# Optimization experiments

Measured on AMD Instinct MI355X. Metric: run time of the kernel, lower is better.

The kernel has to match this reference:

```python
import jax, jax.numpy as jnp
import numpy as np

B, N, L, C, H = 4, 4096, 1024, 1024, 16
D = C // H  # head_dim = 64
SCALE = 1.0 / np.sqrt(D)


def setup_inputs() -> dict:
    key = jax.random.key(0)
    ks = jax.random.split(key, 5)
    return {
        "x": jax.random.normal(ks[0], (B, N, C), dtype=jnp.float32),
        "query": jax.random.normal(ks[1], (B, L, C), dtype=jnp.float32),
        "Wq": jax.random.normal(ks[2], (C, C), dtype=jnp.float32) * 0.02,
        "Wkv": jax.random.normal(ks[3], (2 * C, C), dtype=jnp.float32) * 0.02,
        "Wproj": jax.random.normal(ks[4], (C, C), dtype=jnp.float32) * 0.02,
        "bproj": jnp.zeros((C,), dtype=jnp.float32),
    }


def reference(x, query, Wq, Wkv, Wproj, bproj):
    # q projection: [B,L,C] -> [B,H,L,D]
    q = (query @ Wq.T).reshape(B, L, H, D).transpose(0, 2, 1, 3)
    # kv projection: [B,N,2C] -> k,v each [B,H,N,D]
    kv = (x @ Wkv.T).reshape(B, N, 2, H, D).transpose(2, 0, 3, 1, 4)
    k, v = kv[0], kv[1]
    # unfused SDPA: explicit [B,H,L,N] score matrix (faithful to source)
    attn = jnp.einsum('bhld,bhnd->bhln', q, k) * SCALE
    attn = jax.nn.softmax(attn, axis=-1)
    out = jnp.einsum('bhln,bhnd->bhld', attn, v)  # [B,H,L,D]
    out = out.transpose(0, 2, 1, 3).reshape(B, L, C)
    return out @ Wproj.T + bproj
```

## Files before the change

### kernel.cpp

```cpp
#include <hip/hip_runtime.h>
#include <hip/hip_bf16.h>

typedef __attribute__((ext_vector_type(8))) short short8;
typedef __attribute__((ext_vector_type(4))) float floatx4;

#if __has_builtin(__builtin_amdgcn_exp2f)
#define EXP2(x) __builtin_amdgcn_exp2f(x)
#else
#define EXP2(x) exp2f(x)
#endif

#define BAR() __builtin_amdgcn_s_barrier()
#define FENCE() asm volatile("" ::: "memory")
#define WAIT_LGKM0() asm volatile("s_waitcnt lgkmcnt(0)" ::: "memory")
#define WAIT_VM(n) asm volatile("s_waitcnt vmcnt(" #n ")" ::: "memory")

__device__ __forceinline__ short f2bf(float f) {
  __hip_bfloat16 h = __float2bfloat16(f);
  return *reinterpret_cast<const short*>(&h);
}

__device__ __forceinline__ short8 cvt_f32x8_bf16(const float* __restrict__ p) {
  float4 a = *reinterpret_cast<const float4*>(p);
  float4 b = *reinterpret_cast<const float4*>(p + 4);
  short8 r;
  r[0] = f2bf(a.x); r[1] = f2bf(a.y); r[2] = f2bf(a.z); r[3] = f2bf(a.w);
  r[4] = f2bf(b.x); r[5] = f2bf(b.y); r[6] = f2bf(b.z); r[7] = f2bf(b.w);
  return r;
}

typedef const __attribute__((address_space(1))) void* gptr1;
typedef __attribute__((address_space(3))) void* lptr3;
__device__ __forceinline__ void gl_lds16(const void* g, void* l) {
  __builtin_amdgcn_global_load_lds((gptr1)g, (lptr3)l, 16, 0, 0);
}

__global__ __launch_bounds__(256)
void f32_to_bf16(const float* __restrict__ in, short* __restrict__ out, int n8) {
  int i = blockIdx.x * blockDim.x + threadIdx.x;
  if (i < n8) {
    short8 v = cvt_f32x8_bf16(in + (size_t)i * 8);
    *reinterpret_cast<short8*>(out + (size_t)i * 8) = v;
  }
}

__global__ __launch_bounds__(512, 2)
void gemm256_kv(const short* __restrict__ A, const short* __restrict__ B,
                short* __restrict__ k_out, short* __restrict__ vt,
                int M, int N, int K)
{
  __shared__ __align__(16) short lds[2][2][2][128 * 64];

  const int tid  = threadIdx.x;
  const int lane = tid & 63;
  const int w    = tid >> 6;
  const int wm   = w >> 2;
  const int wn   = w & 3;
  const int cl   = lane & 15;
  const int hi   = lane >> 4;
  const int srl  = lane >> 3;
  const int gch8 = (((lane & 7) ^ srl) << 3);

  const int ntile = N >> 8;
  int bid = blockIdx.x;
  { int cpx = gridDim.x >> 3; bid = (bid & 7) * cpx + (bid >> 3); }
  const int tm = bid / ntile, tn = bid % ntile;
  const int m0 = tm << 8, n0 = tn << 8;
  const int NT = K >> 6;

  auto stageA = [&](int par, int slot, int ktX) {
    #pragma unroll
    for (int j = 0; j < 2; ++j) {
      const int sr = (w << 4) + (j << 3) + srl;
      const int tr = ((sr >> 6) << 7) + (slot << 6) + (sr & 63);
      gl_lds16(A + (size_t)(m0 + tr) * K + ktX + gch8,
               (void*)&lds[par][0][slot][((w << 4) + (j << 3)) * 64]);
    }
  };
  auto stageB = [&](int par, int slot, int ktX) {
    #pragma unroll
    for (int j = 0; j < 2; ++j) {
      const int sr = (w << 4) + (j << 3) + srl;
      const int tr = ((sr >> 5) << 6) + (slot << 5) + (sr & 31);
      gl_lds16(B + (size_t)(n0 + tr) * K + ktX + gch8,
               (void*)&lds[par][1][slot][((w << 4) + (j << 3)) * 64]);
    }
  };

  const floatx4 fzero = {0.f, 0.f, 0.f, 0.f};
  floatx4 acc[8][4];
  #pragma unroll
  for (int m = 0; m < 8; ++m)
    #pragma unroll
    for (int n = 0; n < 4; ++n)
      acc[m][n] = fzero;

  short8 af[4][2], b0[2][2], b1[2][2];

  auto readA = [&](int par, int slot) {
    #pragma unroll
    for (int m = 0; m < 4; ++m)
      #pragma unroll
      for (int ks = 0; ks < 2; ++ks) {
        const int sr = (wm << 6) + (m << 4) + cl;
        const int cpos = ((((ks << 2) + hi) ^ (sr & 7)) << 3);
        af[m][ks] = *reinterpret_cast<const short8*>(&lds[par][0][slot][sr * 64 + cpos]);
      }
  };
  auto readB = [&](int par, int slot, short8 (&bf)[2][2]) {
    #pragma unroll
    for (int n = 0; n < 2; ++n)
      #pragma unroll
      for (int ks = 0; ks < 2; ++ks) {
        const int sr = (wn << 5) + (n << 4) + cl;
        const int cpos = ((((ks << 2) + hi) ^ (sr & 7)) << 3);
        bf[n][ks] = *reinterpret_cast<const short8*>(&lds[par][1][slot][sr * 64 + cpos]);
      }
  };

  #define QUAD(BF, MH, NH)                                                     \
    __builtin_amdgcn_s_setprio(1);                                             \
    _Pragma("unroll")                                                          \
    for (int ks = 0; ks < 2; ++ks)                                             \
      _Pragma("unroll")                                                        \
      for (int m = 0; m < 4; ++m)                                              \
        _Pragma("unroll")                                                      \
        for (int n = 0; n < 2; ++n)                                            \
          acc[(MH)*4 + m][(NH)*2 + n] = __builtin_amdgcn_mfma_f32_16x16x32_bf16( \
              af[m][ks], BF[n][ks], acc[(MH)*4 + m][(NH)*2 + n], 0, 0, 0);     \
    __builtin_amdgcn_s_setprio(0);

  stageA(0, 0, 0); stageB(0, 0, 0); stageB(0, 1, 0); stageA(0, 1, 0);
  stageA(1, 0, 64); stageB(1, 0, 64); stageB(1, 1, 64);
  WAIT_VM(6); BAR(); FENCE();

  for (int t = 0; t < NT; ++t) {
    const int p  = t & 1;
    const int pn = p ^ 1;
    int t1 = t + 1; if (t1 >= NT) t1 -= NT;
    int t2 = t + 2; if (t2 >= NT) t2 -= NT;
    const int kt1 = t1 << 6;
    const int kt2 = t2 << 6;

    readA(p, 0); readB(p, 0, b0);
    stageA(pn, 1, kt1);
    BAR(); WAIT_LGKM0();
    QUAD(b0, 0, 0);
    BAR(); FENCE();

    readB(p, 1, b1);
    stageA(p, 0, kt2);
    BAR(); WAIT_LGKM0();
    QUAD(b1, 0, 1);
    BAR(); FENCE();

    readA(p, 1);
    stageB(p, 0, kt2);
    BAR(); WAIT_LGKM0();
    QUAD(b0, 1, 0);
    BAR(); FENCE();

    stageB(p, 1, kt2);
    WAIT_VM(6);
    BAR(); WAIT_LGKM0();
    QUAD(b1, 1, 1);
    BAR(); FENCE();
  }
  WAIT_VM(0);

  const int rq = hi << 2;
  #pragma unroll
  for (int Mi = 0; Mi < 8; ++Mi) {
    #pragma unroll
    for (int Nn = 0; Nn < 4; ++Nn) {
      const int grow = m0 + wm * 128 + Mi * 16 + rq;
      const int gcol = n0 + wn * 64 + Nn * 16 + cl;
      if (gcol < 1024) {
        #pragma unroll
        for (int i = 0; i < 4; ++i)
          k_out[(size_t)(grow + i) * 1024 + gcol] = f2bf(acc[Mi][Nn][i]);
      } else {
        const int d  = gcol - 1024;
        const int bb = grow >> 12;
        const int nn = grow & 4095;
        size_t base = ((size_t)(bb * 16 + (d >> 6)) * 64 + (d & 63)) * 4096 + nn;
        short4 pk;
        pk.x = f2bf(acc[Mi][Nn][0]); pk.y = f2bf(acc[Mi][Nn][1]);
        pk.z = f2bf(acc[Mi][Nn][2]); pk.w = f2bf(acc[Mi][Nn][3]);
        *reinterpret_cast<short4*>(&vt[base]) = pk;
      }
    }
  }
}

template<int MODE>
__global__ __launch_bounds__(256, 2)
void gemm_bt(const short* __restrict__ A, const short* __restrict__ B,
             void* __restrict__ O0, const float* __restrict__ bias,
             int M, int N, int K, float oscale)
{
  __shared__ short As[128 * 64];
  __shared__ short Bs[128 * 64];

  const int tid  = threadIdx.x;
  const int lane = tid & 63;
  const int w    = tid >> 6;
  const int ntile = N >> 7;
  int bid = blockIdx.x;
  { int cpx = gridDim.x >> 3; bid = (bid & 7) * cpx + (bid >> 3); }
  const int tm = bid / ntile;
  const int tn = bid % ntile;
  const int m0 = tm << 7, n0 = tn << 7;
  const int wr = (w >> 1) << 6;
  const int wc = (w & 1) << 6;

  const int srow = lane >> 3;
  const int scol = (lane & 7) << 3;

  const floatx4 fzero = {0.f, 0.f, 0.f, 0.f};
  floatx4 acc[4][4];
  #pragma unroll
  for (int m = 0; m < 4; ++m)
    #pragma unroll
    for (int n = 0; n < 4; ++n)
      acc[m][n] = fzero;

  for (int kt = 0; kt < K; kt += 64) {
    #pragma unroll
    for (int i = 0; i < 4; ++i) {
      const int chunk = (w << 2) + i;
      const int row   = (chunk << 3) + srow;
      gl_lds16(A + (size_t)(m0 + row) * K + kt + scol, &As[chunk * 512]);
      gl_lds16(B + (size_t)(n0 + row) * K + kt + scol, &Bs[chunk * 512]);
    }
    __syncthreads();

    #pragma unroll
    for (int ks = 0; ks < 2; ++ks) {
      short8 af[4], bfr[4];
      #pragma unroll
      for (int m = 0; m < 4; ++m)
        af[m] = *reinterpret_cast<const short8*>(
            &As[(wr + m * 16 + (lane & 15)) * 64 + ks * 32 + ((lane >> 4) << 3)]);
      #pragma unroll
      for (int n = 0; n < 4; ++n)
        bfr[n] = *reinterpret_cast<const short8*>(
            &Bs[(wc + n * 16 + (lane & 15)) * 64 + ks * 32 + ((lane >> 4) << 3)]);
      #pragma unroll
      for (int m = 0; m < 4; ++m)
        #pragma unroll
        for (int n = 0; n < 4; ++n)
          acc[m][n] = __builtin_amdgcn_mfma_f32_16x16x32_bf16(af[m], bfr[n], acc[m][n], 0, 0, 0);
    }
    __syncthreads();
  }

  const int rq = (lane >> 4) << 2;
  const int cl = lane & 15;
  #pragma unroll
  for (int m = 0; m < 4; ++m) {
    #pragma unroll
    for (int n = 0; n < 4; ++n) {
      const int grow = m0 + wr + m * 16 + rq;
      const int gcol = n0 + wc + n * 16 + cl;
      if (MODE == 0) {
        short* o = (short*)O0;
        #pragma unroll
        for (int i = 0; i < 4; ++i)
          o[(size_t)(grow + i) * N + gcol] = f2bf(acc[m][n][i] * oscale);
      } else {
        float* o = (float*)O0;
        const float bv = bias[gcol];
        #pragma unroll
        for (int i = 0; i < 4; ++i)
          o[(size_t)(grow + i) * N + gcol] = acc[m][n][i] + bv;
      }
    }
  }
}

__global__ __launch_bounds__(256, 2)
void attn_fwd(const short* __restrict__ q_ws, const short* __restrict__ k_ws,
              const short* __restrict__ vt_ws, short* __restrict__ ao_ws)
{
  __shared__ __align__(16) short Ks[2][64 * 64];
  __shared__ __align__(16) short Vts[2][64 * 64];
  __shared__ short Pl[4][32 * 64];

  const int tid  = threadIdx.x;
  const int lane = tid & 63;
  const int w    = tid >> 6;
  const int i    = blockIdx.x;
  const int bh   = (i & 7) * 8 + (i >> 6);
  const int qt   = (i >> 3) & 7;
  const int b  = bh >> 4;
  const int h  = bh & 15;
  const int q0 = qt * 128 + w * 32;
  const int cl = lane & 15;
  const int rq = (lane >> 4) << 2;

  short8 qf[2][2];
  #pragma unroll
  for (int t = 0; t < 2; ++t)
    #pragma unroll
    for (int ks = 0; ks < 2; ++ks) {
      size_t idx = (size_t)(b * 1024 + q0 + t * 16 + cl) * 1024
                 + h * 64 + ks * 32 + ((lane >> 4) << 3);
      qf[t][ks] = *reinterpret_cast<const short8*>(&q_ws[idx]);
    }

  const floatx4 fzero = {0.f, 0.f, 0.f, 0.f};
  floatx4 o[2][4];
  float lr[2] = {0.f, 0.f};
  #pragma unroll
  for (int m = 0; m < 2; ++m)
    #pragma unroll
    for (int nd = 0; nd < 4; ++nd) o[m][nd] = fzero;

  const int c0    = w << 1;
  const int srow8 = lane >> 3;
  const int gch8  = (((lane & 7) ^ srow8) << 3);
  const short* kbase = k_ws + (size_t)(b * 4096 + (c0 << 3) + srow8) * 1024 + h * 64 + gch8;
  const short* vbase = vt_ws + ((size_t)bh * 64 + (c0 << 3) + srow8) * 4096 + gch8;

  auto stage = [&](int buf, int kv0) {
    gl_lds16(kbase + (size_t)kv0 * 1024,          (void*)&Ks[buf][c0 * 512]);
    gl_lds16(kbase + (size_t)kv0 * 1024 + 8192,   (void*)&Ks[buf][(c0 + 1) * 512]);
    gl_lds16(vbase + kv0,                          (void*)&Vts[buf][c0 * 512]);
    gl_lds16(vbase + kv0 + 8 * 4096,               (void*)&Vts[buf][(c0 + 1) * 512]);
  };

  const int hi4   = (lane >> 4) << 2;
  const int pwoff = hi4 & 4;
  const int pwc   = hi4 >> 3;

  stage(0, 0);
  for (int t = 0; t < 64; ++t) {
    const int cur = t & 1;
    const int nt  = (t + 1) & 63;
    stage(cur ^ 1, nt << 6);
    WAIT_VM(4);
    BAR(); FENCE();

    floatx4 s[4][2];
    #pragma unroll
    for (int n = 0; n < 4; ++n)
      #pragma unroll
      for (int tt = 0; tt < 2; ++tt) s[n][tt] = fzero;
    __builtin_amdgcn_s_setprio(1);
    #pragma unroll
    for (int ks = 0; ks < 2; ++ks) {
      short8 kf[4];
      #pragma unroll
      for (int n = 0; n < 4; ++n) {
        int row = n * 16 + cl;
        int ch  = ((ks << 2) + (lane >> 4)) ^ (row & 7);
        kf[n] = *reinterpret_cast<const short8*>(&Ks[cur][row * 64 + (ch << 3)]);
      }
      #pragma unroll
      for (int n = 0; n < 4; ++n)
        #pragma unroll
        for (int tt = 0; tt < 2; ++tt)
          s[n][tt] = __builtin_amdgcn_mfma_f32_16x16x32_bf16(kf[n], qf[tt][ks], s[n][tt], 0, 0, 0);
    }
    __builtin_amdgcn_s_setprio(0);

    #pragma unroll
    for (int tt = 0; tt < 2; ++tt) {
      const int qrow = tt * 16 + cl;
      const int base = qrow * 64;
      const int key  = qrow & 7;
      #pragma unroll
      for (int n = 0; n < 4; ++n) {
        short4 pk;
        #pragma unroll
        for (int ii = 0; ii < 4; ++ii) {
          float p = EXP2(s[n][tt][ii]);
          lr[tt] += p;
          pk[ii] = f2bf(p);
        }
        const int ch = ((n << 1) + pwc) ^ key;
        *reinterpret_cast<short4*>(&Pl[w][base + (ch << 3) + pwoff]) = pk;
      }
    }

    __builtin_amdgcn_s_setprio(1);
    #pragma unroll
    for (int ks = 0; ks < 2; ++ks) {
      short8 pa[2], vf[4];
      #pragma unroll
      for (int m = 0; m < 2; ++m) {
        int row = m * 16 + cl;
        int ch  = ((ks << 2) + (lane >> 4)) ^ (row & 7);
        pa[m] = *reinterpret_cast<const short8*>(&Pl[w][row * 64 + (ch << 3)]);
      }
      #pragma unroll
      for (int nd = 0; nd < 4; ++nd) {
        int row = nd * 16 + cl;
        int ch  = ((ks << 2) + (lane >> 4)) ^ (row & 7);
        vf[nd] = *reinterpret_cast<const short8*>(&Vts[cur][row * 64 + (ch << 3)]);
      }
      #pragma unroll
      for (int m = 0; m < 2; ++m)
        #pragma unroll
        for (int nd = 0; nd < 4; ++nd)
          o[m][nd] = __builtin_amdgcn_mfma_f32_16x16x32_bf16(pa[m], vf[nd], o[m][nd], 0, 0, 0);
    }
    __builtin_amdgcn_s_setprio(0);
    BAR(); FENCE();
  }
  WAIT_VM(0);

  float lf[2];
  #pragma unroll
  for (int t = 0; t < 2; ++t) {
    float l = lr[t];
    l += __shfl_xor(l, 16);
    l += __shfl_xor(l, 32);
    lf[t] = l;
  }
  #pragma unroll
  for (int m = 0; m < 2; ++m) {
    float inv[4];
    #pragma unroll
    for (int ii = 0; ii < 4; ++ii)
      inv[ii] = 1.f / __shfl(lf[m], rq + ii);
    #pragma unroll
    for (int nd = 0; nd < 4; ++nd)
      #pragma unroll
      for (int ii = 0; ii < 4; ++ii) {
        size_t idx = (size_t)(b * 1024 + q0 + m * 16 + rq + ii) * 1024
                   + h * 64 + nd * 16 + cl;
        ao_ws[idx] = f2bf(o[m][nd][ii] * inv[ii]);
      }
  }
}

extern "C" void kernel_launch(void* const* d_in, const int* in_sizes, int n_in,
                              void* d_out, int out_size, void* d_ws, size_t ws_size,
                              hipStream_t stream)
{
  const float* x     = (const float*)d_in[0];
  const float* query = (const float*)d_in[1];
  const float* Wq    = (const float*)d_in[2];
  const float* Wkv   = (const float*)d_in[3];
  const float* Wproj = (const float*)d_in[4];
  const float* bproj = (const float*)d_in[5];
  float* out = (float*)d_out;

  const float QSCALE = 0.18033688011112042f;

  char* ws = (char*)d_ws;
  short* k_ws   = (short*)(ws);
  short* vt_ws  = (short*)(ws + (32ull << 20));
  short* xb     = (short*)(ws + (64ull << 20));
  short* qb     = (short*)(ws + (64ull << 20));
  short* q_ws   = (short*)(ws + (72ull << 20));
  short* ao_ws  = (short*)(ws + (80ull << 20));
  short* wkvb   = (short*)(ws + (96ull << 20));
  short* wqb    = (short*)(ws + (100ull << 20));
  short* wprojb = (short*)(ws + (102ull << 20));

  f32_to_bf16<<<dim3(1024), 256, 0, stream>>>(Wkv,   wkvb,   (2048 * 1024) / 8);
  f32_to_bf16<<<dim3(512),  256, 0, stream>>>(Wq,    wqb,    (1024 * 1024) / 8);
  f32_to_bf16<<<dim3(512),  256, 0, stream>>>(Wproj, wprojb, (1024 * 1024) / 8);
  f32_to_bf16<<<dim3(8192), 256, 0, stream>>>(x,     xb,     (16384 * 1024) / 8);

  gemm256_kv<<<dim3(512), 512, 0, stream>>>(xb, wkvb, k_ws, vt_ws,
                                            16384, 2048, 1024);
  f32_to_bf16<<<dim3(2048), 256, 0, stream>>>(query, qb, (4096 * 1024) / 8);
  gemm_bt<0><<<dim3(256), 256, 0, stream>>>(qb, wqb, q_ws, nullptr,
                                            4096, 1024, 1024, QSCALE);
  attn_fwd<<<dim3(512), 256, 0, stream>>>(q_ws, k_ws, vt_ws, ao_ws);
  gemm_bt<2><<<dim3(256), 256, 0, stream>>>(ao_ws, wprojb, out, bproj,
                                            4096, 1024, 1024, 1.0f);
}
```

Baseline: 234.0 us.

## Halve attention query tile per wave to double grid size and occupancy

Each wave in the attention kernel now handles 16 query rows instead of 32, so a block covers 64 queries and the grid doubles to 1024 blocks. Launch bounds go from 2 to 4 blocks per CU to exploit the smaller register and LDS footprint. The intent is better latency hiding and CU fill. The cost is that every K/V tile is loaded from global memory and LDS twice as often per query row, which lowers arithmetic intensity.

```diff
diff --git a/kernel.cpp b/kernel.cpp
--- a/kernel.cpp
+++ b/kernel.cpp
@@ -279,43 +279,39 @@
   }
 }
 
-__global__ __launch_bounds__(256, 2)
+__global__ __launch_bounds__(256, 4)
 void attn_fwd(const short* __restrict__ q_ws, const short* __restrict__ k_ws,
               const short* __restrict__ vt_ws, short* __restrict__ ao_ws)
 {
   __shared__ __align__(16) short Ks[2][64 * 64];
   __shared__ __align__(16) short Vts[2][64 * 64];
-  __shared__ short Pl[4][32 * 64];
+  __shared__ short Pl[4][16 * 64];
 
   const int tid  = threadIdx.x;
   const int lane = tid & 63;
   const int w    = tid >> 6;
   const int i    = blockIdx.x;
-  const int bh   = (i & 7) * 8 + (i >> 6);
-  const int qt   = (i >> 3) & 7;
+  const int bh   = (i & 7) * 8 + (i >> 7);
+  const int qt   = (i >> 3) & 15;
   const int b  = bh >> 4;
   const int h  = bh & 15;
-  const int q0 = qt * 128 + w * 32;
+  const int q0 = qt * 64 + w * 16;
   const int cl = lane & 15;
   const int rq = (lane >> 4) << 2;
 
-  short8 qf[2][2];
-  #pragma unroll
-  for (int t = 0; t < 2; ++t)
-    #pragma unroll
-    for (int ks = 0; ks < 2; ++ks) {
-      size_t idx = (size_t)(b * 1024 + q0 + t * 16 + cl) * 1024
-                 + h * 64 + ks * 32 + ((lane >> 4) << 3);
-      qf[t][ks] = *reinterpret_cast<const short8*>(&q_ws[idx]);
-    }
+  short8 qf[2];
+  #pragma unroll
+  for (int ks = 0; ks < 2; ++ks) {
+    size_t idx = (size_t)(b * 1024 + q0 + cl) * 1024
+               + h * 64 + ks * 32 + ((lane >> 4) << 3);
+    qf[ks] = *reinterpret_cast<const short8*>(&q_ws[idx]);
+  }
 
   const floatx4 fzero = {0.f, 0.f, 0.f, 0.f};
-  floatx4 o[2][4];
-  float lr[2] = {0.f, 0.f};
-  #pragma unroll
-  for (int m = 0; m < 2; ++m)
-    #pragma unroll
-    for (int nd = 0; nd < 4; ++nd) o[m][nd] = fzero;
+  floatx4 o[4];
+  float lr4[4] = {0.f, 0.f, 0.f, 0.f};
+  #pragma unroll
+  for (int nd = 0; nd < 4; ++nd) o[nd] = fzero;
 
   const int c0    = w << 1;
   const int srow8 = lane >> 3;
@@ -342,11 +338,9 @@
     WAIT_VM(4);
     BAR(); FENCE();
 
-    floatx4 s[4][2];
-    #pragma unroll
-    for (int n = 0; n < 4; ++n)
-      #pragma unroll
-      for (int tt = 0; tt < 2; ++tt) s[n][tt] = fzero;
+    floatx4 s[4];
+    #pragma unroll
+    for (int n = 0; n < 4; ++n) s[n] = fzero;
     __builtin_amdgcn_s_setprio(1);
     #pragma unroll
     for (int ks = 0; ks < 2; ++ks) {
@@ -359,15 +353,12 @@
       }
       #pragma unroll
       for (int n = 0; n < 4; ++n)
-        #pragma unroll
-        for (int tt = 0; tt < 2; ++tt)
-          s[n][tt] = __builtin_amdgcn_mfma_f32_16x16x32_bf16(kf[n], qf[tt][ks], s[n][tt], 0, 0, 0);
+        s[n] = __builtin_amdgcn_mfma_f32_16x16x32_bf16(kf[n], qf[ks], s[n], 0, 0, 0);
     }
     __builtin_amdgcn_s_setprio(0);
 
-    #pragma unroll
-    for (int tt = 0; tt < 2; ++tt) {
-      const int qrow = tt * 16 + cl;
+    {
+      const int qrow = cl;
       const int base = qrow * 64;
       const int key  = qrow & 7;
       #pragma unroll
@@ -375,8 +366,8 @@
         short4 pk;
         #pragma unroll
         for (int ii = 0; ii < 4; ++ii) {
-          float p = EXP2(s[n][tt][ii]);
-          lr[tt] += p;
+          float p = EXP2(s[n][ii]);
+          lr4[n] += p;
           pk[ii] = f2bf(p);
         }
         const int ch = ((n << 1) + pwc) ^ key;
@@ -387,12 +378,11 @@
     __builtin_amdgcn_s_setprio(1);
     #pragma unroll
     for (int ks = 0; ks < 2; ++ks) {
-      short8 pa[2], vf[4];
-      #pragma unroll
-      for (int m = 0; m < 2; ++m) {
-        int row = m * 16 + cl;
+      short8 pa, vf[4];
+      {
+        int row = cl;
         int ch  = ((ks << 2) + (lane >> 4)) ^ (row & 7);
-        pa[m] = *reinterpret_cast<const short8*>(&Pl[w][row * 64 + (ch << 3)]);
+        pa = *reinterpret_cast<const short8*>(&Pl[w][row * 64 + (ch << 3)]);
       }
       #pragma unroll
       for (int nd = 0; nd < 4; ++nd) {
@@ -401,39 +391,33 @@
         vf[nd] = *reinterpret_cast<const short8*>(&Vts[cur][row * 64 + (ch << 3)]);
       }
       #pragma unroll
-      for (int m = 0; m < 2; ++m)
-        #pragma unroll
-        for (int nd = 0; nd < 4; ++nd)
-          o[m][nd] = __builtin_amdgcn_mfma_f32_16x16x32_bf16(pa[m], vf[nd], o[m][nd], 0, 0, 0);
+      for (int nd = 0; nd < 4; ++nd)
+        o[nd] = __builtin_amdgcn_mfma_f32_16x16x32_bf16(pa, vf[nd], o[nd], 0, 0, 0);
     }
     __builtin_amdgcn_s_setprio(0);
     BAR(); FENCE();
   }
   WAIT_VM(0);
 
-  float lf[2];
-  #pragma unroll
-  for (int t = 0; t < 2; ++t) {
-    float l = lr[t];
+  float lf;
+  {
+    float l = (lr4[0] + lr4[1]) + (lr4[2] + lr4[3]);
     l += __shfl_xor(l, 16);
     l += __shfl_xor(l, 32);
-    lf[t] = l;
-  }
-  #pragma unroll
-  for (int m = 0; m < 2; ++m) {
-    float inv[4];
-    #pragma unroll
-    for (int ii = 0; ii < 4; ++ii)
-      inv[ii] = 1.f / __shfl(lf[m], rq + ii);
-    #pragma unroll
-    for (int nd = 0; nd < 4; ++nd)
-      #pragma unroll
-      for (int ii = 0; ii < 4; ++ii) {
-        size_t idx = (size_t)(b * 1024 + q0 + m * 16 + rq + ii) * 1024
-                   + h * 64 + nd * 16 + cl;
-        ao_ws[idx] = f2bf(o[m][nd][ii] * inv[ii]);
-      }
-  }
+    lf = l;
+  }
+  float inv[4];
+  #pragma unroll
+  for (int ii = 0; ii < 4; ++ii)
+    inv[ii] = 1.f / __shfl(lf, rq + ii);
+  #pragma unroll
+  for (int nd = 0; nd < 4; ++nd)
+    #pragma unroll
+    for (int ii = 0; ii < 4; ++ii) {
+      size_t idx = (size_t)(b * 1024 + q0 + rq + ii) * 1024
+                 + h * 64 + nd * 16 + cl;
+      ao_ws[idx] = f2bf(o[nd][ii] * inv[ii]);
+    }
 }
 
 extern "C" void kernel_launch(void* const* d_in, const int* in_sizes, int n_in,
@@ -471,7 +455,7 @@
   f32_to_bf16<<<dim3(2048), 256, 0, stream>>>(query, qb, (4096 * 1024) / 8);
   gemm_bt<0><<<dim3(256), 256, 0, stream>>>(qb, wqb, q_ws, nullptr,
                                             4096, 1024, 1024, QSCALE);
-  attn_fwd<<<dim3(512), 256, 0, stream>>>(q_ws, k_ws, vt_ws, ao_ws);
+  attn_fwd<<<dim3(1024), 256, 0, stream>>>(q_ws, k_ws, vt_ws, ao_ws);
   gemm_bt<2><<<dim3(256), 256, 0, stream>>>(ao_ws, wprojb, out, bproj,
                                             4096, 1024, 1024, 1.0f);
 }
```

New measurement: 241.2 us. 1.03x slower.

## Software-pipeline attention loop to overlap QK of next tile with PV

Applied to the files above, without the earlier changes.

Restructures the attention main loop so the QK^T MFMAs for tile t+1 are issued together with the PV MFMAs for tile t, and the exp/softmax for the next tile runs after the barrier while the next K/V tile loads. P is double-buffered in LDS and swizzled LDS offsets are precomputed once. The intent is to hide the exp/convert latency and loop barriers behind matrix work. In exchange it uses more LDS and registers, adds a full vmcnt(0) wait per iteration, and could lower occupancy.

```diff
diff --git a/kernel.cpp b/kernel.cpp
--- a/kernel.cpp
+++ b/kernel.cpp
@@ -285,7 +285,7 @@
 {
   __shared__ __align__(16) short Ks[2][64 * 64];
   __shared__ __align__(16) short Vts[2][64 * 64];
-  __shared__ short Pl[4][32 * 64];
+  __shared__ __align__(16) short Pl[2][4][32 * 64];
 
   const int tid  = threadIdx.x;
   const int lane = tid & 63;
@@ -297,25 +297,39 @@
   const int h  = bh & 15;
   const int q0 = qt * 128 + w * 32;
   const int cl = lane & 15;
-  const int rq = (lane >> 4) << 2;
+  const int hi = lane >> 4;
+  const int rq = hi << 2;
+  const int key7 = cl & 7;
 
   short8 qf[2][2];
   #pragma unroll
-  for (int t = 0; t < 2; ++t)
+  for (int tt = 0; tt < 2; ++tt)
     #pragma unroll
     for (int ks = 0; ks < 2; ++ks) {
-      size_t idx = (size_t)(b * 1024 + q0 + t * 16 + cl) * 1024
-                 + h * 64 + ks * 32 + ((lane >> 4) << 3);
-      qf[t][ks] = *reinterpret_cast<const short8*>(&q_ws[idx]);
-    }
+      size_t idx = (size_t)(b * 1024 + q0 + tt * 16 + cl) * 1024
+                 + h * 64 + ks * 32 + (hi << 3);
+      qf[tt][ks] = *reinterpret_cast<const short8*>(&q_ws[idx]);
+    }
+
+  int koff[2];
+  #pragma unroll
+  for (int ks = 0; ks < 2; ++ks)
+    koff[ks] = cl * 64 + ((((ks << 2) + hi) ^ key7) << 3);
+  const int pwc   = hi >> 1;
+  const int pwoff = (hi & 1) << 2;
+  int pwch[4];
+  #pragma unroll
+  for (int n = 0; n < 4; ++n)
+    pwch[n] = ((((n << 1) + pwc) ^ key7) << 3) + pwoff + cl * 64;
 
   const floatx4 fzero = {0.f, 0.f, 0.f, 0.f};
   floatx4 o[2][4];
-  float lr[2] = {0.f, 0.f};
-  #pragma unroll
-  for (int m = 0; m < 2; ++m)
-    #pragma unroll
-    for (int nd = 0; nd < 4; ++nd) o[m][nd] = fzero;
+  floatx4 s[4][2];
+  float lr[2][2] = {{0.f, 0.f}, {0.f, 0.f}};
+  #pragma unroll
+  for (int tt = 0; tt < 2; ++tt)
+    #pragma unroll
+    for (int nd = 0; nd < 4; ++nd) o[tt][nd] = fzero;
 
   const int c0    = w << 1;
   const int srow8 = lane >> 3;
@@ -330,94 +344,91 @@
     gl_lds16(vbase + kv0 + 8 * 4096,               (void*)&Vts[buf][(c0 + 1) * 512]);
   };
 
-  const int hi4   = (lane >> 4) << 2;
-  const int pwoff = hi4 & 4;
-  const int pwc   = hi4 >> 3;
-
-  stage(0, 0);
-  for (int t = 0; t < 64; ++t) {
-    const int cur = t & 1;
-    const int nt  = (t + 1) & 63;
-    stage(cur ^ 1, nt << 6);
-    WAIT_VM(4);
-    BAR(); FENCE();
-
-    floatx4 s[4][2];
+  auto zs = [&]() {
     #pragma unroll
     for (int n = 0; n < 4; ++n)
       #pragma unroll
       for (int tt = 0; tt < 2; ++tt) s[n][tt] = fzero;
-    __builtin_amdgcn_s_setprio(1);
+  };
+  auto qk = [&](const short* kb) {
     #pragma unroll
     for (int ks = 0; ks < 2; ++ks) {
       short8 kf[4];
       #pragma unroll
-      for (int n = 0; n < 4; ++n) {
-        int row = n * 16 + cl;
-        int ch  = ((ks << 2) + (lane >> 4)) ^ (row & 7);
-        kf[n] = *reinterpret_cast<const short8*>(&Ks[cur][row * 64 + (ch << 3)]);
-      }
+      for (int n = 0; n < 4; ++n)
+        kf[n] = *reinterpret_cast<const short8*>(kb + koff[ks] + n * 1024);
       #pragma unroll
       for (int n = 0; n < 4; ++n)
         #pragma unroll
         for (int tt = 0; tt < 2; ++tt)
           s[n][tt] = __builtin_amdgcn_mfma_f32_16x16x32_bf16(kf[n], qf[tt][ks], s[n][tt], 0, 0, 0);
     }
-    __builtin_amdgcn_s_setprio(0);
-
-    #pragma unroll
-    for (int tt = 0; tt < 2; ++tt) {
-      const int qrow = tt * 16 + cl;
-      const int base = qrow * 64;
-      const int key  = qrow & 7;
+  };
+  auto pv = [&](const short* plb, const short* vb) {
+    #pragma unroll
+    for (int ks = 0; ks < 2; ++ks) {
+      short8 pa[2], vf[4];
+      #pragma unroll
+      for (int tt = 0; tt < 2; ++tt)
+        pa[tt] = *reinterpret_cast<const short8*>(plb + koff[ks] + tt * 1024);
+      #pragma unroll
+      for (int nd = 0; nd < 4; ++nd)
+        vf[nd] = *reinterpret_cast<const short8*>(vb + koff[ks] + nd * 1024);
+      #pragma unroll
+      for (int tt = 0; tt < 2; ++tt)
+        #pragma unroll
+        for (int nd = 0; nd < 4; ++nd)
+          o[tt][nd] = __builtin_amdgcn_mfma_f32_16x16x32_bf16(pa[tt], vf[nd], o[tt][nd], 0, 0, 0);
+    }
+  };
+  auto smax = [&](short* plw) {
+    #pragma unroll
+    for (int tt = 0; tt < 2; ++tt)
       #pragma unroll
       for (int n = 0; n < 4; ++n) {
         short4 pk;
         #pragma unroll
         for (int ii = 0; ii < 4; ++ii) {
           float p = EXP2(s[n][tt][ii]);
-          lr[tt] += p;
+          lr[tt][n & 1] += p;
           pk[ii] = f2bf(p);
         }
-        const int ch = ((n << 1) + pwc) ^ key;
-        *reinterpret_cast<short4*>(&Pl[w][base + (ch << 3) + pwoff]) = pk;
-      }
-    }
-
+        *reinterpret_cast<short4*>(plw + tt * 1024 + pwch[n]) = pk;
+      }
+  };
+
+  stage(0, 0);
+  WAIT_VM(0); BAR(); FENCE();
+  zs(); qk(&Ks[0][0]);
+  stage(1, 64);
+  smax(&Pl[0][w][0]);
+  int pb = 0;
+
+  for (int t = 0; t < 63; ++t) {
+    const int cur = t & 1;
+    WAIT_VM(0); BAR(); FENCE();
     __builtin_amdgcn_s_setprio(1);
-    #pragma unroll
-    for (int ks = 0; ks < 2; ++ks) {
-      short8 pa[2], vf[4];
-      #pragma unroll
-      for (int m = 0; m < 2; ++m) {
-        int row = m * 16 + cl;
-        int ch  = ((ks << 2) + (lane >> 4)) ^ (row & 7);
-        pa[m] = *reinterpret_cast<const short8*>(&Pl[w][row * 64 + (ch << 3)]);
-      }
-      #pragma unroll
-      for (int nd = 0; nd < 4; ++nd) {
-        int row = nd * 16 + cl;
-        int ch  = ((ks << 2) + (lane >> 4)) ^ (row & 7);
-        vf[nd] = *reinterpret_cast<const short8*>(&Vts[cur][row * 64 + (ch << 3)]);
-      }
-      #pragma unroll
-      for (int m = 0; m < 2; ++m)
-        #pragma unroll
-        for (int nd = 0; nd < 4; ++nd)
-          o[m][nd] = __builtin_amdgcn_mfma_f32_16x16x32_bf16(pa[m], vf[nd], o[m][nd], 0, 0, 0);
-    }
+    zs();
+    qk(&Ks[cur ^ 1][0]);
+    pv(&Pl[pb][w][0], &Vts[cur][0]);
     __builtin_amdgcn_s_setprio(0);
-    BAR(); FENCE();
-  }
+    FENCE(); BAR();
+    stage(cur, ((t + 2) & 63) << 6);
+    smax(&Pl[pb ^ 1][w][0]);
+    pb ^= 1;
+  }
+  __builtin_amdgcn_s_setprio(1);
+  pv(&Pl[pb][w][0], &Vts[1][0]);
+  __builtin_amdgcn_s_setprio(0);
   WAIT_VM(0);
 
   float lf[2];
   #pragma unroll
-  for (int t = 0; t < 2; ++t) {
-    float l = lr[t];
+  for (int tt = 0; tt < 2; ++tt) {
+    float l = lr[tt][0] + lr[tt][1];
     l += __shfl_xor(l, 16);
     l += __shfl_xor(l, 32);
-    lf[t] = l;
+    lf[tt] = l;
   }
   #pragma unroll
   for (int m = 0; m < 2; ++m) {
```

Result: faster. 224.0 us (-4.3%).
